# Kernel optimization log

Measured on AMD Instinct MI355X. Metric: run time of the kernel, lower is better.

## Reference

```python
import jax, jax.numpy as jnp
import numpy as np

N_NODES = 100000
N_EDGES = 1000000
VOCAB = 128
EMB = 64
HID = 64
N_CLASSES = 2
N_GRAPHS = 2048


def setup_inputs() -> dict:
    key = jax.random.key(0)
    ks = jax.random.split(key, 12)
    x = jax.random.randint(ks[0], (N_NODES,), 0, VOCAB)
    edge_index = jax.random.randint(ks[1], (2, N_EDGES), 0, N_NODES)
    batch = jnp.sort(jax.random.randint(ks[2], (N_NODES,), 0, N_GRAPHS))

    def glorot(k, shape):
        fan = shape[0]
        return jax.random.normal(k, shape, dtype=jnp.float32) / np.sqrt(fan).astype(np.float32)

    emb = jax.random.normal(ks[3], (VOCAB, EMB), dtype=jnp.float32)
    W1_l = glorot(ks[4], (EMB, HID)); b1 = jnp.zeros((HID,), jnp.float32)
    W1_r = glorot(ks[5], (EMB, HID))
    W2_l = glorot(ks[6], (HID, HID)); b2 = jnp.zeros((HID,), jnp.float32)
    W2_r = glorot(ks[7], (HID, HID))
    W_out = glorot(ks[8], (HID, N_CLASSES)); b_out = jnp.zeros((N_CLASSES,), jnp.float32)
    return {"x": x, "edge_index": edge_index, "batch": batch, "emb": emb,
            "W1_l": W1_l, "b1": b1, "W1_r": W1_r,
            "W2_l": W2_l, "b2": b2, "W2_r": W2_r,
            "W_out": W_out, "b_out": b_out}


def _sage_conv(h, src, dst, Wl, bl, Wr):
    # PyG SAGEConv: out = lin_l(mean_{j in N(i)} h_j) + lin_r(h_i); lin_r has no bias
    msgs = h[src]                                                        # [E, D] gather
    agg = jax.ops.segment_sum(msgs, dst, num_segments=N_NODES)          # [N, D] scatter-add
    cnt = jax.ops.segment_sum(jnp.ones((src.shape[0], 1), h.dtype), dst,
                              num_segments=N_NODES)                      # [N, 1] degree
    mean = agg / jnp.maximum(cnt, 1.0)
    return mean @ Wl + bl + h @ Wr


def reference(x, edge_index, batch, emb, W1_l, b1, W1_r, W2_l, b2, W2_r, W_out, b_out):
    src, dst = edge_index[0], edge_index[1]
    h = emb[x]                                                           # [N, EMB]
    h = jax.nn.relu(_sage_conv(h, src, dst, W1_l, b1, W1_r))             # [N, HID]
    h = jax.nn.relu(_sage_conv(h, src, dst, W2_l, b2, W2_r))             # [N, HID]
    # global_mean_pool over graph ids
    gsum = jax.ops.segment_sum(h, batch, num_segments=N_GRAPHS)          # [G, HID]
    gcnt = jax.ops.segment_sum(jnp.ones((N_NODES, 1), h.dtype), batch,
                               num_segments=N_GRAPHS)
    pooled = gsum / jnp.maximum(gcnt, 1.0)
    return pooled @ W_out + b_out                                        # [G, C]
```

## Files before the change

kernel.cpp:

```cpp
#include <hip/hip_runtime.h>
#include <hip/hip_bf16.h>

#define N_NODES 100000
#define N_EDGES 1000000
#define EMB 64
#define HID 64
#define VOCAB 128
#define N_GRAPHS 2048

#define CBUCKET 256
#define NBK ((N_NODES + CBUCKET - 1) / CBUCKET)
#define CAP 4096
#define CHUNK 4096
#define SCAT_BLOCKS ((N_EDGES + CHUNK - 1) / CHUNK)
#define GB ((N_NODES + 255) / 256)

#define BCASTF(v, l) __int_as_float(__builtin_amdgcn_readlane(__float_as_int(v), (l)))

typedef __attribute__((ext_vector_type(8))) short short8;
typedef __attribute__((ext_vector_type(4))) float f32x4;
typedef __attribute__((ext_vector_type(2))) float f32x2;

__device__ __forceinline__ float bf2f(unsigned short u) {
    return __uint_as_float((unsigned)u << 16);
}
__device__ __forceinline__ unsigned short f2bf(float f) {
    return __bfloat16_as_ushort(__float2bfloat16(f));
}

__global__ __launch_bounds__(256) void scatter_kernel(
    const int* __restrict__ src, const int* __restrict__ dst,
    const int* __restrict__ x,
    int* __restrict__ cursor, unsigned* __restrict__ edge8,
    const int* __restrict__ batch, int* __restrict__ gstart,
    const float* __restrict__ emb, const float* __restrict__ W1l,
    const float* __restrict__ W1r,
    const float* __restrict__ W2l, const float* __restrict__ W2r,
    float* __restrict__ embW1l, float* __restrict__ embW1r,
    unsigned short* __restrict__ w2frag, unsigned char* __restrict__ p8z)
{
    __shared__ unsigned earr[CHUNK];
    __shared__ unsigned short karr[CHUNK];
    __shared__ int bcnt[NBK];
    __shared__ int bbase[NBK];
    int b = blockIdx.x;
    int t = threadIdx.x;

    if (b < SCAT_BLOCKS) {
        for (int i = t; i < NBK; i += 256) bcnt[i] = 0;
        __syncthreads();
        int e0 = b * CHUNK;
        int n = min(e0 + CHUNK, N_EDGES) - e0;
        for (int i = t; i < n; i += 256) {
            int d = dst[e0 + i];
            int s = src[e0 + i];
            int xv = x[s];
            int k = d >> 8;
            earr[i] = (unsigned)s | ((unsigned)xv << 17) | ((unsigned)(d & 255) << 24);
            karr[i] = (unsigned short)k;
            atomicAdd(&bcnt[k], 1);
        }
        __syncthreads();
        for (int i = t; i < NBK; i += 256) {
            int c = bcnt[i];
            bbase[i] = i * CAP + (c ? atomicAdd(&cursor[i], c) : 0);
            bcnt[i] = 0;
        }
        __syncthreads();
        for (int i = t; i < n; i += 256) {
            int k = karr[i];
            int off = atomicAdd(&bcnt[k], 1);
            edge8[bbase[k] + off] = earr[i];
        }
    } else if (b < SCAT_BLOCKS + GB) {
        int i = (b - SCAT_BLOCKS) * 256 + t;
        if (i >= N_NODES) return;
        int bg = batch[i];
        int bp = (i == 0) ? -1 : batch[i - 1];
        for (int g = bp + 1; g <= bg; ++g) gstart[g] = i;
        if (i == N_NODES - 1)
            for (int g = bg + 1; g <= N_GRAPHS; ++g) gstart[g] = N_NODES;
    } else {
        int vb = b - SCAT_BLOCKS - GB;
        if (vb == 0 && t < 16)
            ((unsigned*)(p8z + (size_t)N_NODES * 64))[t] = 0u;
        int wave = t >> 6, lane = t & 63;
        int v = vb * 4 + wave;
        if (v < VOCAB) {
            float er = emb[v * 64 + lane];
            float al = 0.f, ar = 0.f;
#pragma unroll 8
            for (int d = 0; d < 64; ++d) {
                float e = BCASTF(er, d);
                al += e * W1l[d * 64 + lane];
                ar += e * W1r[d * 64 + lane];
            }
            embW1l[v * 64 + lane] = al;
            embW1r[v * 64 + lane] = ar;
        }
        int g = vb * 256 + t;
        int j = g & 7, l = (g >> 3) & 63, h = (g >> 9) & 1, tt = g >> 10;
        int k = h * 32 + ((l >> 4) * 8) + j;
        int n = tt * 16 + (l & 15);
        float w = (n < 64) ? W2l[k * 64 + n] : W2r[k * 64 + (n - 64)];
        w2frag[g] = f2bf(w);
    }
}

__global__ __launch_bounds__(256) void csr_kernel(
    const unsigned* __restrict__ edge8, const int* __restrict__ cursor,
    int* __restrict__ row_start, int* __restrict__ deg, int* __restrict__ col,
    const float* __restrict__ embW1l, const float* __restrict__ embW1r,
    unsigned short* __restrict__ w1frag)
{
    __shared__ int cnt[CBUCKET];
    __shared__ int scn[CBUCKET];
    int b = blockIdx.x;
    int t = threadIdx.x;

    if (b < 8) {
        int g0 = (b * 256 + t) * 8;
#pragma unroll
        for (int j = 0; j < 8; ++j) {
            int g = g0 + j;
            int fi = g >> 9;
            int kf = fi >> 2, nt = fi & 3;
            int l = (g >> 3) & 63, jj = g & 7;
            int kg = kf * 32 + ((l >> 4) << 3) + jj;
            int n = nt * 16 + (l & 15);
            float w = (kg < 128) ? embW1l[kg * 64 + n] : embW1r[(kg - 128) * 64 + n];
            w1frag[g] = f2bf(w);
        }
    }

    int lo = b * CAP, hi = lo + cursor[b];
    cnt[t] = 0;
    __syncthreads();
    for (int i = lo + t; i < hi; i += 256)
        atomicAdd(&cnt[edge8[i] >> 24], 1);
    __syncthreads();
    int v = cnt[t];
    scn[t] = v;
    __syncthreads();
    for (int off = 1; off < 256; off <<= 1) {
        int tmp = (t >= off) ? scn[t - off] : 0;
        __syncthreads();
        scn[t] += tmp;
        __syncthreads();
    }
    int excl = scn[t] - v;
    int node = b * CBUCKET + t;
    if (node < N_NODES) { row_start[node] = lo + excl; deg[node] = v; }
    cnt[t] = excl;
    __syncthreads();
    for (int i = lo + t; i < hi; i += 256) {
        unsigned e = edge8[i];
        int slot = atomicAdd(&cnt[e >> 24], 1);
        col[lo + slot] = (int)(e & 0xFFFFFF);
    }
}

__global__ __launch_bounds__(256) void sage1_kernel(
    const int* __restrict__ x, const int* __restrict__ deg,
    const unsigned* __restrict__ edge8, const int* __restrict__ cursor,
    const unsigned short* __restrict__ w1frag,
    const unsigned short* __restrict__ w2frag, const float* __restrict__ b1,
    unsigned char* __restrict__ p8, unsigned short* __restrict__ q16)
{
    __shared__ unsigned hist[128 * 32];
    __shared__ unsigned short msbuf[128 * 72];
    __shared__ int xl[128];
    __shared__ float invd[128];

    int blk = blockIdx.x, bucket = blk >> 1, half = blk & 1;
    int t = threadIdx.x;
    int nbase = bucket * CBUCKET + half * 128;

    for (int i = t * 4; i < 128 * 32; i += 1024)
        *(uint4*)&hist[i] = (uint4){0u, 0u, 0u, 0u};
    if (t < 128) {
        int node = nbase + t;
        int dv = (node < N_NODES) ? deg[node] : 0;
        invd[t] = 1.0f / fmaxf((float)dv, 1.0f);
        xl[t] = (node < N_NODES) ? x[node] : 0;
    }
    __syncthreads();

    int lo = bucket * CAP, ecnt = cursor[bucket];
    for (int i = t; i < ecnt; i += 256) {
        unsigned e = edge8[lo + i];
        int ld = (int)(e >> 24);
        if ((ld >> 7) == half) {
            int r = ld & 127;
            int xv = (int)((e >> 17) & 127);
            int wc = (xv >> 2) ^ ((r & 7) << 2);
            atomicAdd(&hist[r * 32 + wc], 1u << ((xv & 3) * 8));
        }
    }
    __syncthreads();

    int wave = t >> 6, lane = t & 63;
    int m = lane & 15;
    int qd = lane >> 4;
    int hswz = (m & 7) << 2;

#pragma unroll
    for (int rt = wave * 2; rt < wave * 2 + 2; ++rt) {
        short8 acnt[4], aself[4];
#pragma unroll
        for (int kf = 0; kf < 4; ++kf) {
            int w0 = (kf * 8 + qd * 2) ^ hswz;
            uint2 u = *(const uint2*)&hist[(rt * 16 + m) * 32 + w0];
            short8 f;
            f[0] = (short)f2bf((float)(u.x & 255));
            f[1] = (short)f2bf((float)((u.x >> 8) & 255));
            f[2] = (short)f2bf((float)((u.x >> 16) & 255));
            f[3] = (short)f2bf((float)(u.x >> 24));
            f[4] = (short)f2bf((float)(u.y & 255));
            f[5] = (short)f2bf((float)((u.y >> 8) & 255));
            f[6] = (short)f2bf((float)((u.y >> 16) & 255));
            f[7] = (short)f2bf((float)(u.y >> 24));
            acnt[kf] = f;
        }
        int xv = xl[rt * 16 + m];
#pragma unroll
        for (int kf = 0; kf < 4; ++kf) {
            int v = xv - kf * 32 - qd * 8;
            short8 f;
#pragma unroll
            for (int j = 0; j < 8; ++j)
                f[j] = (v == j) ? (short)0x3F80 : (short)0;
            aself[kf] = f;
        }
        float iv0 = invd[rt * 16 + qd * 4 + 0];
        float iv1 = invd[rt * 16 + qd * 4 + 1];
        float iv2 = invd[rt * 16 + qd * 4 + 2];
        float iv3 = invd[rt * 16 + qd * 4 + 3];

#pragma unroll
        for (int nt = 0; nt < 4; ++nt) {
            f32x4 accA = {0.f, 0.f, 0.f, 0.f};
            f32x4 accS = {0.f, 0.f, 0.f, 0.f};
#pragma unroll
            for (int kf = 0; kf < 4; ++kf) {
                short8 bA = *(const short8*)(w1frag + ((kf * 4 + nt) * 64 + lane) * 8);
                accA = __builtin_amdgcn_mfma_f32_16x16x32_bf16(acnt[kf], bA, accA, 0, 0, 0);
            }
#pragma unroll
            for (int kf = 0; kf < 4; ++kf) {
                short8 bS = *(const short8*)(w1frag + (((kf + 4) * 4 + nt) * 64 + lane) * 8);
                accS = __builtin_amdgcn_mfma_f32_16x16x32_bf16(aself[kf], bS, accS, 0, 0, 0);
            }
            int c = nt * 16 + m;
            float b1c = b1[c];
            int rb = rt * 16 + qd * 4;
            msbuf[(rb + 0) * 72 + c] = f2bf(fmaxf(accA[0] * iv0 + accS[0] + b1c, 0.f));
            msbuf[(rb + 1) * 72 + c] = f2bf(fmaxf(accA[1] * iv1 + accS[1] + b1c, 0.f));
            msbuf[(rb + 2) * 72 + c] = f2bf(fmaxf(accA[2] * iv2 + accS[2] + b1c, 0.f));
            msbuf[(rb + 3) * 72 + c] = f2bf(fmaxf(accA[3] * iv3 + accS[3] + b1c, 0.f));
        }
    }
    __syncthreads();

#pragma unroll
    for (int rt = wave * 2; rt < wave * 2 + 2; ++rt) {
        const unsigned short* arow = &msbuf[(rt * 16 + m) * 72 + qd * 8];
        short8 a0 = *(const short8*)(arow);
        short8 a1 = *(const short8*)(arow + 32);
        int rowb = nbase + rt * 16 + qd * 4;

#pragma unroll
        for (int tt = 0; tt < 8; ++tt) {
            short8 b0 = *(const short8*)(w2frag + tt * 1024 + lane * 8);
            short8 b1v = *(const short8*)(w2frag + tt * 1024 + 512 + lane * 8);
            f32x4 acc = {0.f, 0.f, 0.f, 0.f};
            acc = __builtin_amdgcn_mfma_f32_16x16x32_bf16(a0, b0, acc, 0, 0, 0);
            acc = __builtin_amdgcn_mfma_f32_16x16x32_bf16(a1, b1v, acc, 0, 0, 0);
            int o = tt * 16 + m;
            if (o < 64) {
                int pk01 = __builtin_amdgcn_cvt_pk_fp8_f32(acc[0], acc[1], 0, false);
                int pk23 = __builtin_amdgcn_cvt_pk_fp8_f32(acc[2], acc[3], 0, false);
                if (rowb + 0 < N_NODES) p8[(rowb + 0) * 64 + o] = (unsigned char)(pk01 & 0xff);
                if (rowb + 1 < N_NODES) p8[(rowb + 1) * 64 + o] = (unsigned char)((pk01 >> 8) & 0xff);
                if (rowb + 2 < N_NODES) p8[(rowb + 2) * 64 + o] = (unsigned char)(pk23 & 0xff);
                if (rowb + 3 < N_NODES) p8[(rowb + 3) * 64 + o] = (unsigned char)((pk23 >> 8) & 0xff);
            } else {
                int oc = o & 63;
#pragma unroll
                for (int i = 0; i < 4; ++i)
                    if (rowb + i < N_NODES)
                        q16[(rowb + i) * 64 + oc] = f2bf(acc[i]);
            }
        }
    }
}

#define S2_NPW 8
#define ZROW N_NODES
__global__ __launch_bounds__(256, 4) void sage2_kernel(
    const unsigned char* __restrict__ p, const unsigned short* __restrict__ q,
    const int* __restrict__ row_start, const int* __restrict__ deg,
    const int* __restrict__ col, const float* __restrict__ b2,
    const float* __restrict__ Wout, const int* __restrict__ batch,
    float* __restrict__ gsum)
{
    int t = threadIdx.x;
    int wave = t >> 6, lane = t & 63;
    int base_node = (blockIdx.x * 4 + wave) * S2_NPW;
    int c = lane & 15;
    int g = lane >> 4;

    float4 b2v = ((const float4*)b2)[c];
    float4 w01 = ((const float4*)Wout)[c * 2];
    float4 w23 = ((const float4*)Wout)[c * 2 + 1];

    int rs[S2_NPW], dgs[S2_NPW], cidx[S2_NPW];
#pragma unroll
    for (int n = 0; n < S2_NPW; ++n) {
        rs[n] = row_start[base_node + n];
        dgs[n] = deg[base_node + n];
    }
#pragma unroll
    for (int n = 0; n < S2_NPW; ++n)
        cidx[n] = (lane < dgs[n]) ? (col[rs[n] + lane] & 0x1FFFF) : ZROW;

    unsigned vv[S2_NPW][4];
    ushort4 qv[S2_NPW];
#pragma unroll
    for (int n = 0; n < S2_NPW; ++n) {
        int i0 = __shfl(cidx[n], g, 64);
        int i1 = __shfl(cidx[n], 4 + g, 64);
        int i2 = __shfl(cidx[n], 8 + g, 64);
        int i3 = __shfl(cidx[n], 12 + g, 64);
        vv[n][0] = *(const unsigned*)(p + (size_t)i0 * 64 + c * 4);
        vv[n][1] = *(const unsigned*)(p + (size_t)i1 * 64 + c * 4);
        vv[n][2] = *(const unsigned*)(p + (size_t)i2 * 64 + c * 4);
        vv[n][3] = *(const unsigned*)(p + (size_t)i3 * 64 + c * 4);
    }
#pragma unroll
    for (int n = 0; n < S2_NPW; ++n)
        qv[n] = *(const ushort4*)(q + (size_t)(base_node + n) * 64 + c * 4);

#define ACC(a, v) { f32x2 f01_ = __builtin_amdgcn_cvt_pk_f32_fp8((int)(v), false); \
                    f32x2 f23_ = __builtin_amdgcn_cvt_pk_f32_fp8((int)(v), true);  \
                    (a).x += f01_.x; (a).y += f01_.y; (a).z += f23_.x; (a).w += f23_.y; }

#pragma unroll
    for (int n = 0; n < S2_NPW; n += 2) {
        int dgA = dgs[n], dgB = dgs[n + 1];

        float4 aA = {0.f,0.f,0.f,0.f}, aB = {0.f,0.f,0.f,0.f};
        ACC(aA, vv[n][0])     ACC(aA, vv[n][1])     ACC(aA, vv[n][2])     ACC(aA, vv[n][3])
        ACC(aB, vv[n + 1][0]) ACC(aB, vv[n + 1][1]) ACC(aB, vv[n + 1][2]) ACC(aB, vv[n + 1][3])

        for (int j = 16; j < dgA; j += 8) {
            int i0 = __shfl(cidx[n], j + g, 64);
            int i1 = __shfl(cidx[n], j + 4 + g, 64);
            unsigned v0 = *(const unsigned*)(p + (size_t)i0 * 64 + c * 4);
            unsigned v1 = *(const unsigned*)(p + (size_t)i1 * 64 + c * 4);
            ACC(aA, v0) ACC(aA, v1)
        }
        for (int j = 16; j < dgB; j += 8) {
            int i0 = __shfl(cidx[n + 1], j + g, 64);
            int i1 = __shfl(cidx[n + 1], j + 4 + g, 64);
            unsigned v0 = *(const unsigned*)(p + (size_t)i0 * 64 + c * 4);
            unsigned v1 = *(const unsigned*)(p + (size_t)i1 * 64 + c * 4);
            ACC(aB, v0) ACC(aB, v1)
        }
        for (int k = 64; k < dgA; ++k) {
            int r = col[rs[n] + k] & 0x1FFFF;
            unsigned v = *(const unsigned*)(p + (size_t)r * 64 + c * 4);
            if (g == 0) ACC(aA, v)
        }
        for (int k = 64; k < dgB; ++k) {
            int r = col[rs[n + 1] + k] & 0x1FFFF;
            unsigned v = *(const unsigned*)(p + (size_t)r * 64 + c * 4);
            if (g == 0) ACC(aB, v)
        }

        aA.x += __shfl_xor(aA.x, 16, 64); aA.y += __shfl_xor(aA.y, 16, 64);
        aA.z += __shfl_xor(aA.z, 16, 64); aA.w += __shfl_xor(aA.w, 16, 64);
        aB.x += __shfl_xor(aB.x, 16, 64); aB.y += __shfl_xor(aB.y, 16, 64);
        aB.z += __shfl_xor(aB.z, 16, 64); aB.w += __shfl_xor(aB.w, 16, 64);
        aA.x += __shfl_xor(aA.x, 32, 64); aA.y += __shfl_xor(aA.y, 32, 64);
        aA.z += __shfl_xor(aA.z, 32, 64); aA.w += __shfl_xor(aA.w, 32, 64);
        aB.x += __shfl_xor(aB.x, 32, 64); aB.y += __shfl_xor(aB.y, 32, 64);
        aB.z += __shfl_xor(aB.z, 32, 64); aB.w += __shfl_xor(aB.w, 32, 64);

#pragma unroll
        for (int e = 0; e < 2; ++e) {
            int node = base_node + n + e;
            int dg = (e == 0) ? dgA : dgB;
            float4 a = (e == 0) ? aA : aB;
            ushort4 qvv = qv[n + e];
            float inv = 1.0f / fmaxf((float)dg, 1.0f);
            float h0 = fmaxf(a.x * inv + b2v.x + bf2f(qvv.x), 0.f);
            float h1 = fmaxf(a.y * inv + b2v.y + bf2f(qvv.y), 0.f);
            float h2 = fmaxf(a.z * inv + b2v.z + bf2f(qvv.z), 0.f);
            float h3 = fmaxf(a.w * inv + b2v.w + bf2f(qvv.w), 0.f);

            float p0 = h0 * w01.x + h1 * w01.z + h2 * w23.x + h3 * w23.z;
            float p1 = h0 * w01.y + h1 * w01.w + h2 * w23.y + h3 * w23.w;
            if (g != 0) { p0 = 0.f; p1 = 0.f; }
            p0 += __shfl_down(p0, 8, 64);  p1 += __shfl_down(p1, 8, 64);
            p0 += __shfl_down(p0, 4, 64);  p1 += __shfl_down(p1, 4, 64);
            p0 += __shfl_down(p0, 2, 64);  p1 += __shfl_down(p1, 2, 64);
            p0 += __shfl_down(p0, 1, 64);  p1 += __shfl_down(p1, 1, 64);
            if (lane == 0) {
                int grp = batch[node];
                atomicAdd(&gsum[grp * 2 + 0], p0);
                atomicAdd(&gsum[grp * 2 + 1], p1);
            }
        }
    }
#undef ACC
}

__global__ __launch_bounds__(256) void finalize_kernel(
    const float* __restrict__ gsum, const int* __restrict__ gstart,
    const float* __restrict__ bout, float* __restrict__ out)
{
    int g = blockIdx.x * 256 + threadIdx.x;
    if (g >= N_GRAPHS) return;
    int cnt = gstart[g + 1] - gstart[g];
    float inv = 1.0f / fmaxf((float)cnt, 1.0f);
    out[g * 2 + 0] = gsum[g * 2 + 0] * inv + bout[0];
    out[g * 2 + 1] = gsum[g * 2 + 1] * inv + bout[1];
}

extern "C" void kernel_launch(void* const* d_in, const int* in_sizes, int n_in,
                              void* d_out, int out_size, void* d_ws, size_t ws_size,
                              hipStream_t stream) {
    const int*   x    = (const int*)  d_in[0];
    const int*   ei   = (const int*)  d_in[1];
    const int*   batch= (const int*)  d_in[2];
    const float* emb  = (const float*)d_in[3];
    const float* W1l  = (const float*)d_in[4];
    const float* b1   = (const float*)d_in[5];
    const float* W1r  = (const float*)d_in[6];
    const float* W2l  = (const float*)d_in[7];
    const float* b2   = (const float*)d_in[8];
    const float* W2r  = (const float*)d_in[9];
    const float* Wout = (const float*)d_in[10];
    const float* bout = (const float*)d_in[11];
    float* out = (float*)d_out;

    const int* src = ei;
    const int* dst = ei + N_EDGES;

    char* ws = (char*)d_ws;
    size_t off = 0;
    unsigned char*  p8     = (unsigned char*) (ws + off); off += (size_t)N_NODES * 64 + 64;
    unsigned short* q16    = (unsigned short*)(ws + off); off += (size_t)N_NODES * 64 * 2;
    unsigned short* w2frag = (unsigned short*)(ws + off); off += (size_t)8192 * 2;
    unsigned short* w1frag = (unsigned short*)(ws + off); off += (size_t)16384 * 2;
    float*    embW1l = (float*)   (ws + off); off += (size_t)VOCAB * 64 * 4;
    float*    embW1r = (float*)   (ws + off); off += (size_t)VOCAB * 64 * 4;
    int*      rowst  = (int*)     (ws + off); off += (size_t)N_NODES * 4;
    int*      deg    = (int*)     (ws + off); off += (size_t)N_NODES * 4;
    int*      col    = (int*)     (ws + off); off += (size_t)(NBK * CAP + 256) * 4;
    unsigned* edge8  = (unsigned*)(ws + off); off += (size_t)NBK * CAP * 4;
    int*      gstart = (int*)     (ws + off); off += (size_t)(N_GRAPHS + 1) * 4;
    int*      cursor = (int*)     (ws + off); off += (size_t)NBK * 4;
    float*    gsum   = (float*)   (ws + off); off += (size_t)N_GRAPHS * 2 * 4;

    hipMemsetAsync(cursor, 0, (size_t)NBK * 4 + (size_t)N_GRAPHS * 2 * 4, stream);

    scatter_kernel<<<SCAT_BLOCKS + GB + 32, 256, 0, stream>>>(
        src, dst, x, cursor, edge8,
        batch, gstart, emb, W1l, W1r, W2l, W2r, embW1l, embW1r, w2frag, p8);
    csr_kernel<<<NBK, 256, 0, stream>>>(edge8, cursor, rowst, deg, col,
                                        embW1l, embW1r, w1frag);
    sage1_kernel<<<NBK * 2, 256, 0, stream>>>(
        x, deg, edge8, cursor, w1frag, w2frag, b1, p8, q16);
    sage2_kernel<<<N_NODES / (4 * S2_NPW), 256, 0, stream>>>(
        p8, q16, rowst, deg, col, b2, Wout, batch, gsum);
    finalize_kernel<<<(N_GRAPHS + 255) / 256, 256, 0, stream>>>(gsum, gstart, bout, out);
}
```

Baseline: 214.3 us.

## Precompute padded 16-wide neighbor index table for sage2 gathers

Adds a kernel that writes the first 16 neighbor indices of each node into a fixed-stride padded table (missing slots point at a zero row). sage2 then loads those indices directly per lane instead of reading the CSR row and broadcasting with shuffles, and only falls back to the CSR row for nodes with degree above 16. The aim is to cut the index-load-then-shuffle dependency chain and get the feature gathers issued sooner. The cost is an extra kernel launch and a 6.4 MB table written and read back. The launch_bounds occupancy hint is also dropped and sched barriers are added.

```diff
diff --git a/kernel.cpp b/kernel.cpp
--- a/kernel.cpp
+++ b/kernel.cpp
@@ -160,6 +160,18 @@
     }
 }
 
+#define ZROW N_NODES
+__global__ __launch_bounds__(256) void col16_kernel(
+    const int* __restrict__ row_start, const int* __restrict__ deg,
+    const int* __restrict__ col, int* __restrict__ col16)
+{
+    int node = blockIdx.x * 16 + (threadIdx.x >> 4);
+    int j = threadIdx.x & 15;
+    if (node >= N_NODES) return;
+    int d = deg[node];
+    col16[node * 16 + j] = (j < d) ? (col[row_start[node] + j] & 0x1FFFF) : ZROW;
+}
+
 __global__ __launch_bounds__(256) void sage1_kernel(
     const int* __restrict__ x, const int* __restrict__ deg,
     const unsigned* __restrict__ edge8, const int* __restrict__ cursor,
@@ -296,11 +308,11 @@
 }
 
 #define S2_NPW 8
-#define ZROW N_NODES
-__global__ __launch_bounds__(256, 4) void sage2_kernel(
+__global__ __launch_bounds__(256) void sage2_kernel(
     const unsigned char* __restrict__ p, const unsigned short* __restrict__ q,
     const int* __restrict__ row_start, const int* __restrict__ deg,
-    const int* __restrict__ col, const float* __restrict__ b2,
+    const int* __restrict__ col, const int* __restrict__ col16,
+    const float* __restrict__ b2,
     const float* __restrict__ Wout, const int* __restrict__ batch,
     float* __restrict__ gsum)
 {
@@ -314,32 +326,35 @@
     float4 w01 = ((const float4*)Wout)[c * 2];
     float4 w23 = ((const float4*)Wout)[c * 2 + 1];
 
-    int rs[S2_NPW], dgs[S2_NPW], cidx[S2_NPW];
+    int dgs[S2_NPW];
+#pragma unroll
+    for (int n = 0; n < S2_NPW; ++n)
+        dgs[n] = deg[base_node + n];
+
+    int idx[S2_NPW][4];
 #pragma unroll
     for (int n = 0; n < S2_NPW; ++n) {
-        rs[n] = row_start[base_node + n];
-        dgs[n] = deg[base_node + n];
-    }
-#pragma unroll
-    for (int n = 0; n < S2_NPW; ++n)
-        cidx[n] = (lane < dgs[n]) ? (col[rs[n] + lane] & 0x1FFFF) : ZROW;
+        const int* cp = col16 + (size_t)(base_node + n) * 16 + g;
+        idx[n][0] = cp[0];
+        idx[n][1] = cp[4];
+        idx[n][2] = cp[8];
+        idx[n][3] = cp[12];
+    }
+    __builtin_amdgcn_sched_barrier(0);
 
     unsigned vv[S2_NPW][4];
     ushort4 qv[S2_NPW];
 #pragma unroll
     for (int n = 0; n < S2_NPW; ++n) {
-        int i0 = __shfl(cidx[n], g, 64);
-        int i1 = __shfl(cidx[n], 4 + g, 64);
-        int i2 = __shfl(cidx[n], 8 + g, 64);
-        int i3 = __shfl(cidx[n], 12 + g, 64);
-        vv[n][0] = *(const unsigned*)(p + (size_t)i0 * 64 + c * 4);
-        vv[n][1] = *(const unsigned*)(p + (size_t)i1 * 64 + c * 4);
-        vv[n][2] = *(const unsigned*)(p + (size_t)i2 * 64 + c * 4);
-        vv[n][3] = *(const unsigned*)(p + (size_t)i3 * 64 + c * 4);
+        vv[n][0] = *(const unsigned*)(p + (size_t)idx[n][0] * 64 + c * 4);
+        vv[n][1] = *(const unsigned*)(p + (size_t)idx[n][1] * 64 + c * 4);
+        vv[n][2] = *(const unsigned*)(p + (size_t)idx[n][2] * 64 + c * 4);
+        vv[n][3] = *(const unsigned*)(p + (size_t)idx[n][3] * 64 + c * 4);
     }
 #pragma unroll
     for (int n = 0; n < S2_NPW; ++n)
         qv[n] = *(const ushort4*)(q + (size_t)(base_node + n) * 64 + c * 4);
+    __builtin_amdgcn_sched_barrier(0);
 
 #define ACC(a, v) { f32x2 f01_ = __builtin_amdgcn_cvt_pk_f32_fp8((int)(v), false); \
                     f32x2 f23_ = __builtin_amdgcn_cvt_pk_f32_fp8((int)(v), true);  \
@@ -353,29 +368,27 @@
         ACC(aA, vv[n][0])     ACC(aA, vv[n][1])     ACC(aA, vv[n][2])     ACC(aA, vv[n][3])
         ACC(aB, vv[n + 1][0]) ACC(aB, vv[n + 1][1]) ACC(aB, vv[n + 1][2]) ACC(aB, vv[n + 1][3])
 
-        for (int j = 16; j < dgA; j += 8) {
-            int i0 = __shfl(cidx[n], j + g, 64);
-            int i1 = __shfl(cidx[n], j + 4 + g, 64);
-            unsigned v0 = *(const unsigned*)(p + (size_t)i0 * 64 + c * 4);
-            unsigned v1 = *(const unsigned*)(p + (size_t)i1 * 64 + c * 4);
-            ACC(aA, v0) ACC(aA, v1)
-        }
-        for (int j = 16; j < dgB; j += 8) {
-            int i0 = __shfl(cidx[n + 1], j + g, 64);
-            int i1 = __shfl(cidx[n + 1], j + 4 + g, 64);
-            unsigned v0 = *(const unsigned*)(p + (size_t)i0 * 64 + c * 4);
-            unsigned v1 = *(const unsigned*)(p + (size_t)i1 * 64 + c * 4);
-            ACC(aB, v0) ACC(aB, v1)
-        }
-        for (int k = 64; k < dgA; ++k) {
-            int r = col[rs[n] + k] & 0x1FFFF;
-            unsigned v = *(const unsigned*)(p + (size_t)r * 64 + c * 4);
-            if (g == 0) ACC(aA, v)
-        }
-        for (int k = 64; k < dgB; ++k) {
-            int r = col[rs[n + 1] + k] & 0x1FFFF;
-            unsigned v = *(const unsigned*)(p + (size_t)r * 64 + c * 4);
-            if (g == 0) ACC(aB, v)
+        if (dgA > 16) {
+            int rsA = row_start[base_node + n];
+            for (int j = 16; j < dgA; j += 8) {
+                int r0 = j + g, r1 = j + 4 + g;
+                int i0 = (r0 < dgA) ? (col[rsA + r0] & 0x1FFFF) : ZROW;
+                int i1 = (r1 < dgA) ? (col[rsA + r1] & 0x1FFFF) : ZROW;
+                unsigned v0 = *(const unsigned*)(p + (size_t)i0 * 64 + c * 4);
+                unsigned v1 = *(const unsigned*)(p + (size_t)i1 * 64 + c * 4);
+                ACC(aA, v0) ACC(aA, v1)
+            }
+        }
+        if (dgB > 16) {
+            int rsB = row_start[base_node + n + 1];
+            for (int j = 16; j < dgB; j += 8) {
+                int r0 = j + g, r1 = j + 4 + g;
+                int i0 = (r0 < dgB) ? (col[rsB + r0] & 0x1FFFF) : ZROW;
+                int i1 = (r1 < dgB) ? (col[rsB + r1] & 0x1FFFF) : ZROW;
+                unsigned v0 = *(const unsigned*)(p + (size_t)i0 * 64 + c * 4);
+                unsigned v1 = *(const unsigned*)(p + (size_t)i1 * 64 + c * 4);
+                ACC(aB, v0) ACC(aB, v1)
+            }
         }
 
         aA.x += __shfl_xor(aA.x, 16, 64); aA.y += __shfl_xor(aA.y, 16, 64);
@@ -459,6 +472,7 @@
     int*      rowst  = (int*)     (ws + off); off += (size_t)N_NODES * 4;
     int*      deg    = (int*)     (ws + off); off += (size_t)N_NODES * 4;
     int*      col    = (int*)     (ws + off); off += (size_t)(NBK * CAP + 256) * 4;
+    int*      col16  = (int*)     (ws + off); off += (size_t)(N_NODES + 16) * 16 * 4;
     unsigned* edge8  = (unsigned*)(ws + off); off += (size_t)NBK * CAP * 4;
     int*      gstart = (int*)     (ws + off); off += (size_t)(N_GRAPHS + 1) * 4;
     int*      cursor = (int*)     (ws + off); off += (size_t)NBK * 4;
@@ -471,9 +485,10 @@
         batch, gstart, emb, W1l, W1r, W2l, W2r, embW1l, embW1r, w2frag, p8);
     csr_kernel<<<NBK, 256, 0, stream>>>(edge8, cursor, rowst, deg, col,
                                         embW1l, embW1r, w1frag);
+    col16_kernel<<<(N_NODES + 15) / 16, 256, 0, stream>>>(rowst, deg, col, col16);
     sage1_kernel<<<NBK * 2, 256, 0, stream>>>(
         x, deg, edge8, cursor, w1frag, w2frag, b1, p8, q16);
     sage2_kernel<<<N_NODES / (4 * S2_NPW), 256, 0, stream>>>(
-        p8, q16, rowst, deg, col, b2, Wout, batch, gsum);
+        p8, q16, rowst, deg, col, col16, b2, Wout, batch, gsum);
     finalize_kernel<<<(N_GRAPHS + 255) / 256, 256, 0, stream>>>(gsum, gstart, bout, out);
 }
```

Result: slower. 226.3 us (+5.6%).
